# Performance work log

Measured on AMD Instinct MI355X. Metric: run time of the kernel, lower is better.

## Reference

```python
import jax, jax.numpy as jnp
import numpy as np

N_NODES = 100000
IN_DIM = 64
HIDDEN = 128
N_EDGES = 1000000


def _linear_params(key, fan_in, fan_out):
    # torch nn.Linear default init: U(-1/sqrt(fan_in), 1/sqrt(fan_in))
    kW, kb = jax.random.split(key)
    bound = 1.0 / np.sqrt(fan_in)
    W = jax.random.uniform(kW, (fan_in, fan_out), jnp.float32, -bound, bound)
    b = jax.random.uniform(kb, (fan_out,), jnp.float32, -bound, bound)
    return W, b


def setup_inputs() -> dict:
    key = jax.random.key(0)
    kx, ke, k1, k2, k3, k4 = jax.random.split(key, 6)
    x = jax.random.normal(kx, (N_NODES, IN_DIM), jnp.float32)
    edge_index = jax.random.randint(ke, (2, N_EDGES), 0, N_NODES, jnp.int64)
    W1, b1 = _linear_params(k1, IN_DIM * 2, HIDDEN)
    W2, b2 = _linear_params(k2, HIDDEN, HIDDEN)
    W3, b3 = _linear_params(k3, HIDDEN, HIDDEN)
    W4, b4 = _linear_params(k4, HIDDEN, 1)
    return {"x": x, "edge_index": edge_index,
            "W1": W1, "b1": b1, "W2": W2, "b2": b2,
            "W3": W3, "b3": b3, "W4": W4, "b4": b4}


def reference(x, edge_index, W1, b1, W2, b2, W3, b3, W4, b4):
    src, dst = edge_index[0], edge_index[1]
    # [E, 2*in_dim] gathered edge inputs
    edge_inputs = jnp.concatenate([x[src], x[dst]], axis=1)
    h = jnp.tanh(edge_inputs @ W1 + b1)
    h = jnp.tanh(h @ W2 + b2)
    h = jnp.tanh(h @ W3 + b3)
    out = jax.nn.sigmoid(h @ W4 + b4)
    return out.squeeze(-1)  # [E]
```

## Files before the change

kernel.cpp:

```cpp
#include <hip/hip_runtime.h>
#include <cstdint>

typedef _Float16 f16x8 __attribute__((ext_vector_type(8)));
typedef float    f32x4 __attribute__((ext_vector_type(4)));

#define E_TOTAL   1000000
#define N_NODES   100000
#define NROUNDS   3907
#define GRID_MAIN 512

__device__ __forceinline__ float fast_tanh(float x) {
  float e = __builtin_amdgcn_exp2f(x * 2.8853900817779268f);
  return 1.0f - 2.0f * __builtin_amdgcn_rcpf(1.0f + e);
}
__device__ __forceinline__ float fast_sigmoid(float x) {
  float e = __builtin_amdgcn_exp2f(x * -1.4426950408889634f);
  return __builtin_amdgcn_rcpf(1.0f + e);
}
__device__ __forceinline__ uint32_t pack2(float a, float b) {
  return __builtin_bit_cast(uint32_t, __builtin_amdgcn_cvt_pkrtz(a, b));
}
__device__ __forceinline__ f16x8 asfrag(const uint32_t (&u)[4]) {
  uint4 v;
  v.x = u[0]; v.y = u[1]; v.z = u[2]; v.w = u[3];
  return __builtin_bit_cast(f16x8, v);
}

__global__ void kconv_x(const float* __restrict__ x, _Float16* __restrict__ xh) {
  int i = blockIdx.x * 256 + threadIdx.x;
  if (i >= (N_NODES * 64) / 8) return;
  const float4* p = (const float4*)x + (size_t)i * 2;
  float4 a = p[0], b = p[1];
  f16x8 o = {(_Float16)a.x, (_Float16)a.y, (_Float16)a.z, (_Float16)a.w,
             (_Float16)b.x, (_Float16)b.y, (_Float16)b.z, (_Float16)b.w};
  *((f16x8*)xh + i) = o;
}

__global__ void kswz_w(const float* __restrict__ W1, const float* __restrict__ W2,
                       const float* __restrict__ W3, _Float16* __restrict__ wswz) {
  int idx = blockIdx.x * 256 + threadIdx.x;
  if (idx >= 49152) return;
  int jj = idx & 7;
  int l  = (idx >> 3) & 63;
  int s  = (idx >> 9) & 3;
  int T  = (idx >> 11) & 7;
  int L  = idx >> 14;
  int k  = 32 * s + 4 * (l >> 4) + (jj & 3) + 16 * (jj >> 2);
  int n  = 16 * T + (l & 15);
  const float* W = (L == 0) ? W1 : ((L == 1) ? W2 : W3);
  wswz[idx] = (_Float16)W[k * 128 + n];
}

template <int L>
__device__ __forceinline__ void mlp_layer(const _Float16* lds_w, const float* lds_b,
                                          int lane,
                                          const uint32_t (&Bin)[2][4][4],
                                          uint32_t (&Bout)[2][4][4]) {
  const int g = lane >> 4;
#pragma unroll
  for (int T = 0; T < 8; ++T) {
    const f32x4 bf = *(const f32x4*)(lds_b + L * 128 + T * 16 + g * 4);
    f32x4 acc0 = bf, acc1 = bf;
#pragma unroll
    for (int s = 0; s < 4; ++s) {
      const f16x8 W = *(const f16x8*)(lds_w + (size_t)(((L * 8 + T) * 4 + s) * 512) + lane * 8);
      acc0 = __builtin_amdgcn_mfma_f32_16x16x32_f16(W, asfrag(Bin[0][s]), acc0, 0, 0, 0);
      acc1 = __builtin_amdgcn_mfma_f32_16x16x32_f16(W, asfrag(Bin[1][s]), acc1, 0, 0, 0);
    }
    const int si = T >> 1, d = (T & 1) * 2;
    Bout[0][si][d]     = pack2(fast_tanh(acc0[0]), fast_tanh(acc0[1]));
    Bout[0][si][d + 1] = pack2(fast_tanh(acc0[2]), fast_tanh(acc0[3]));
    Bout[1][si][d]     = pack2(fast_tanh(acc1[0]), fast_tanh(acc1[1]));
    Bout[1][si][d + 1] = pack2(fast_tanh(acc1[2]), fast_tanh(acc1[3]));
  }
}

__device__ __forceinline__ void mlp_out(const _Float16* __restrict__ gw3,
                                        const float* lds_b,
                                        int lane,
                                        const uint32_t (&Bin)[2][4][4],
                                        float (&dot)[2]) {
  const int g = lane >> 4;
  dot[0] = dot[1] = 0.f;
#pragma unroll
  for (int T = 0; T < 8; ++T) {
    const f32x4 bf = *(const f32x4*)(lds_b + 256 + T * 16 + g * 4);
    const f32x4 wf = *(const f32x4*)(lds_b + 384 + T * 16 + g * 4);
    f32x4 acc0 = bf, acc1 = bf;
#pragma unroll
    for (int s = 0; s < 4; ++s) {
      const f16x8 W = *(const f16x8*)(gw3 + (size_t)((T * 4 + s) * 512) + lane * 8);
      acc0 = __builtin_amdgcn_mfma_f32_16x16x32_f16(W, asfrag(Bin[0][s]), acc0, 0, 0, 0);
      acc1 = __builtin_amdgcn_mfma_f32_16x16x32_f16(W, asfrag(Bin[1][s]), acc1, 0, 0, 0);
    }
    dot[0] += fast_tanh(acc0[0]) * wf[0] + fast_tanh(acc0[1]) * wf[1]
            + fast_tanh(acc0[2]) * wf[2] + fast_tanh(acc0[3]) * wf[3];
    dot[1] += fast_tanh(acc1[0]) * wf[0] + fast_tanh(acc1[1]) * wf[1]
            + fast_tanh(acc1[2]) * wf[2] + fast_tanh(acc1[3]) * wf[3];
  }
}

template <bool XH>
__global__ __launch_bounds__(512)
void edge_mlp(
    const int* __restrict__ eidx,
    const _Float16* __restrict__ xh,
    const float* __restrict__ xf,
    const _Float16* __restrict__ wswz,
    const float* __restrict__ b1, const float* __restrict__ b2,
    const float* __restrict__ b3, const float* __restrict__ w4,
    const float* __restrict__ b4g,
    float* __restrict__ out) {
  extern __shared__ char smem[];
  _Float16* lds_w = (_Float16*)smem;
  float*    lds_b = (float*)(smem + 65536);
  const _Float16* gw3 = wswz + 32768;

  const int tid = threadIdx.x;
  {
    const uint4* src = (const uint4*)wswz;
    uint4* dst = (uint4*)smem;
#pragma unroll
    for (int i = 0; i < 8; ++i) dst[tid + i * 512] = src[tid + i * 512];
  }
  if (tid < 128) {
    lds_b[tid]       = b1[tid];
    lds_b[128 + tid] = b2[tid];
    lds_b[256 + tid] = b3[tid];
    lds_b[384 + tid] = w4[tid];
  }
  __syncthreads();

  const float b4v = b4g[0];
  const int wid = tid >> 6, lane = tid & 63;
  const int c = lane & 15, g = lane >> 4;

  for (int round = blockIdx.x; round < NROUNDS; round += GRID_MAIN) {
    const int ebase = round * 256 + wid * 32;

    uint32_t B0[2][4][4];
#pragma unroll
    for (int t = 0; t < 2; ++t) {
      int e  = ebase + t * 16 + c;
      int ee = (e < E_TOTAL) ? e : 0;
      int sN = eidx[ee];
      int dN = eidx[E_TOTAL + ee];
      if (XH) {
        const _Float16* ps = xh + (size_t)sN * 64 + g * 4;
        const _Float16* pd = xh + (size_t)dN * 64 + g * 4;
#pragma unroll
        for (int sp = 0; sp < 2; ++sp) {
#pragma unroll
          for (int h = 0; h < 2; ++h) {
            uint2 rs = *(const uint2*)(ps + sp * 32 + h * 16);
            uint2 rd = *(const uint2*)(pd + sp * 32 + h * 16);
            B0[t][sp][h * 2]         = rs.x;
            B0[t][sp][h * 2 + 1]     = rs.y;
            B0[t][2 + sp][h * 2]     = rd.x;
            B0[t][2 + sp][h * 2 + 1] = rd.y;
          }
        }
      } else {
        const float* ps = xf + (size_t)sN * 64 + g * 4;
        const float* pd = xf + (size_t)dN * 64 + g * 4;
#pragma unroll
        for (int sp = 0; sp < 2; ++sp) {
#pragma unroll
          for (int h = 0; h < 2; ++h) {
            float4 fs = *(const float4*)(ps + sp * 32 + h * 16);
            float4 fd = *(const float4*)(pd + sp * 32 + h * 16);
            B0[t][sp][h * 2]         = pack2(fs.x, fs.y);
            B0[t][sp][h * 2 + 1]     = pack2(fs.z, fs.w);
            B0[t][2 + sp][h * 2]     = pack2(fd.x, fd.y);
            B0[t][2 + sp][h * 2 + 1] = pack2(fd.z, fd.w);
          }
        }
      }
    }

    uint32_t B1r[2][4][4], B2r[2][4][4];
    mlp_layer<0>(lds_w, lds_b, lane, B0, B1r);
    mlp_layer<1>(lds_w, lds_b, lane, B1r, B2r);

    float dot[2];
    mlp_out(gw3, lds_b, lane, B2r, dot);

#pragma unroll
    for (int t = 0; t < 2; ++t) {
      float v = dot[t];
      v += __shfl_xor(v, 16);
      v += __shfl_xor(v, 32);
      dot[t] = v;
    }
    if (g == 0) {
#pragma unroll
      for (int t = 0; t < 2; ++t) {
        int e = ebase + t * 16 + c;
        if (e < E_TOTAL) out[e] = fast_sigmoid(dot[t] + b4v);
      }
    }
    __builtin_amdgcn_sched_barrier(0);
  }
}

extern "C" void kernel_launch(void* const* d_in, const int* in_sizes, int n_in,
                              void* d_out, int out_size, void* d_ws, size_t ws_size,
                              hipStream_t stream) {
  (void)in_sizes; (void)n_in; (void)out_size;
  const float* x  = (const float*)d_in[0];
  const int* eidx = (const int*)d_in[1];
  const float* W1 = (const float*)d_in[2];
  const float* b1 = (const float*)d_in[3];
  const float* W2 = (const float*)d_in[4];
  const float* b2 = (const float*)d_in[5];
  const float* W3 = (const float*)d_in[6];
  const float* b3 = (const float*)d_in[7];
  const float* w4 = (const float*)d_in[8];
  const float* b4 = (const float*)d_in[9];
  float* out = (float*)d_out;

  const size_t XH_BYTES   = (size_t)N_NODES * 64 * 2;
  const size_t WS_W_BYTES = 49152 * 2;
  const bool xh_ok = ws_size >= XH_BYTES + WS_W_BYTES;

  _Float16* ws_xh = (_Float16*)d_ws;
  _Float16* ws_w  = (_Float16*)((char*)d_ws + (xh_ok ? XH_BYTES : 0));

  kswz_w<<<192, 256, 0, stream>>>(W1, W2, W3, ws_w);
  if (xh_ok) kconv_x<<<3125, 256, 0, stream>>>(x, ws_xh);

  const size_t lds_bytes = 65536 + 2048;
  if (xh_ok) {
    edge_mlp<true><<<GRID_MAIN, 512, lds_bytes, stream>>>(
        eidx, ws_xh, x, ws_w, b1, b2, b3, w4, b4, out);
  } else {
    edge_mlp<false><<<GRID_MAIN, 512, lds_bytes, stream>>>(
        eidx, ws_xh, x, ws_w, b1, b2, b3, w4, b4, out);
  }
}
```

Measured before the change: 164.0 us.

## Fold tanh scale into weights, halve block size, stream W2 from global

The tanh input scale factor is folded into the swizzled fp16 weights and the biases, so each activation skips one multiply. Blocks shrink from 512 to 256 threads and the grid doubles. LDS now holds only W1 (32KB), and W2 is read from global/L2 the way W3 already was, to fit more blocks per CU. The risk is that per-tile W2 loads from L2 cost more than the occupancy gain, and fp16 rounding of the prescaled weights changes slightly.

```diff
diff --git a/kernel.cpp b/kernel.cpp
--- a/kernel.cpp
+++ b/kernel.cpp
@@ -6,11 +6,12 @@
 
 #define E_TOTAL   1000000
 #define N_NODES   100000
-#define NROUNDS   3907
-#define GRID_MAIN 512
-
-__device__ __forceinline__ float fast_tanh(float x) {
-  float e = __builtin_amdgcn_exp2f(x * 2.8853900817779268f);
+#define NROUNDS   7813
+#define GRID_MAIN 1024
+#define SCL       2.8853900817779268f
+
+__device__ __forceinline__ float tanh_pre(float a) {
+  float e = __builtin_amdgcn_exp2f(a);
   return 1.0f - 2.0f * __builtin_amdgcn_rcpf(1.0f + e);
 }
 __device__ __forceinline__ float fast_sigmoid(float x) {
@@ -48,12 +49,12 @@
   int k  = 32 * s + 4 * (l >> 4) + (jj & 3) + 16 * (jj >> 2);
   int n  = 16 * T + (l & 15);
   const float* W = (L == 0) ? W1 : ((L == 1) ? W2 : W3);
-  wswz[idx] = (_Float16)W[k * 128 + n];
+  wswz[idx] = (_Float16)(W[k * 128 + n] * SCL);
 }
 
 template <int L>
-__device__ __forceinline__ void mlp_layer(const _Float16* lds_w, const float* lds_b,
-                                          int lane,
+__device__ __forceinline__ void mlp_layer(const _Float16* __restrict__ w,
+                                          const float* lds_b, int lane,
                                           const uint32_t (&Bin)[2][4][4],
                                           uint32_t (&Bout)[2][4][4]) {
   const int g = lane >> 4;
@@ -63,21 +64,20 @@
     f32x4 acc0 = bf, acc1 = bf;
 #pragma unroll
     for (int s = 0; s < 4; ++s) {
-      const f16x8 W = *(const f16x8*)(lds_w + (size_t)(((L * 8 + T) * 4 + s) * 512) + lane * 8);
+      const f16x8 W = *(const f16x8*)(w + (size_t)(((T * 4 + s)) * 512) + lane * 8);
       acc0 = __builtin_amdgcn_mfma_f32_16x16x32_f16(W, asfrag(Bin[0][s]), acc0, 0, 0, 0);
       acc1 = __builtin_amdgcn_mfma_f32_16x16x32_f16(W, asfrag(Bin[1][s]), acc1, 0, 0, 0);
     }
     const int si = T >> 1, d = (T & 1) * 2;
-    Bout[0][si][d]     = pack2(fast_tanh(acc0[0]), fast_tanh(acc0[1]));
-    Bout[0][si][d + 1] = pack2(fast_tanh(acc0[2]), fast_tanh(acc0[3]));
-    Bout[1][si][d]     = pack2(fast_tanh(acc1[0]), fast_tanh(acc1[1]));
-    Bout[1][si][d + 1] = pack2(fast_tanh(acc1[2]), fast_tanh(acc1[3]));
+    Bout[0][si][d]     = pack2(tanh_pre(acc0[0]), tanh_pre(acc0[1]));
+    Bout[0][si][d + 1] = pack2(tanh_pre(acc0[2]), tanh_pre(acc0[3]));
+    Bout[1][si][d]     = pack2(tanh_pre(acc1[0]), tanh_pre(acc1[1]));
+    Bout[1][si][d + 1] = pack2(tanh_pre(acc1[2]), tanh_pre(acc1[3]));
   }
 }
 
 __device__ __forceinline__ void mlp_out(const _Float16* __restrict__ gw3,
-                                        const float* lds_b,
-                                        int lane,
+                                        const float* lds_b, int lane,
                                         const uint32_t (&Bin)[2][4][4],
                                         float (&dot)[2]) {
   const int g = lane >> 4;
@@ -93,15 +93,15 @@
       acc0 = __builtin_amdgcn_mfma_f32_16x16x32_f16(W, asfrag(Bin[0][s]), acc0, 0, 0, 0);
       acc1 = __builtin_amdgcn_mfma_f32_16x16x32_f16(W, asfrag(Bin[1][s]), acc1, 0, 0, 0);
     }
-    dot[0] += fast_tanh(acc0[0]) * wf[0] + fast_tanh(acc0[1]) * wf[1]
-            + fast_tanh(acc0[2]) * wf[2] + fast_tanh(acc0[3]) * wf[3];
-    dot[1] += fast_tanh(acc1[0]) * wf[0] + fast_tanh(acc1[1]) * wf[1]
-            + fast_tanh(acc1[2]) * wf[2] + fast_tanh(acc1[3]) * wf[3];
+    dot[0] += tanh_pre(acc0[0]) * wf[0] + tanh_pre(acc0[1]) * wf[1]
+            + tanh_pre(acc0[2]) * wf[2] + tanh_pre(acc0[3]) * wf[3];
+    dot[1] += tanh_pre(acc1[0]) * wf[0] + tanh_pre(acc1[1]) * wf[1]
+            + tanh_pre(acc1[2]) * wf[2] + tanh_pre(acc1[3]) * wf[3];
   }
 }
 
 template <bool XH>
-__global__ __launch_bounds__(512)
+__global__ __launch_bounds__(256)
 void edge_mlp(
     const int* __restrict__ eidx,
     const _Float16* __restrict__ xh,
@@ -112,8 +112,9 @@
     const float* __restrict__ b4g,
     float* __restrict__ out) {
   extern __shared__ char smem[];
-  _Float16* lds_w = (_Float16*)smem;
-  float*    lds_b = (float*)(smem + 65536);
+  _Float16* lds_w1 = (_Float16*)smem;
+  float*    lds_b  = (float*)(smem + 32768);
+  const _Float16* gw2 = wswz + 16384;
   const _Float16* gw3 = wswz + 32768;
 
   const int tid = threadIdx.x;
@@ -121,12 +122,12 @@
     const uint4* src = (const uint4*)wswz;
     uint4* dst = (uint4*)smem;
 #pragma unroll
-    for (int i = 0; i < 8; ++i) dst[tid + i * 512] = src[tid + i * 512];
+    for (int i = 0; i < 8; ++i) dst[tid + i * 256] = src[tid + i * 256];
   }
   if (tid < 128) {
-    lds_b[tid]       = b1[tid];
-    lds_b[128 + tid] = b2[tid];
-    lds_b[256 + tid] = b3[tid];
+    lds_b[tid]       = b1[tid] * SCL;
+    lds_b[128 + tid] = b2[tid] * SCL;
+    lds_b[256 + tid] = b3[tid] * SCL;
     lds_b[384 + tid] = w4[tid];
   }
   __syncthreads();
@@ -136,7 +137,7 @@
   const int c = lane & 15, g = lane >> 4;
 
   for (int round = blockIdx.x; round < NROUNDS; round += GRID_MAIN) {
-    const int ebase = round * 256 + wid * 32;
+    const int ebase = round * 128 + wid * 32;
 
     uint32_t B0[2][4][4];
 #pragma unroll
@@ -179,8 +180,8 @@
     }
 
     uint32_t B1r[2][4][4], B2r[2][4][4];
-    mlp_layer<0>(lds_w, lds_b, lane, B0, B1r);
-    mlp_layer<1>(lds_w, lds_b, lane, B1r, B2r);
+    mlp_layer<0>(lds_w1, lds_b, lane, B0, B1r);
+    mlp_layer<1>(gw2,    lds_b, lane, B1r, B2r);
 
     float dot[2];
     mlp_out(gw3, lds_b, lane, B2r, dot);
@@ -229,12 +230,12 @@
   kswz_w<<<192, 256, 0, stream>>>(W1, W2, W3, ws_w);
   if (xh_ok) kconv_x<<<3125, 256, 0, stream>>>(x, ws_xh);
 
-  const size_t lds_bytes = 65536 + 2048;
+  const size_t lds_bytes = 32768 + 2048;
   if (xh_ok) {
-    edge_mlp<true><<<GRID_MAIN, 512, lds_bytes, stream>>>(
+    edge_mlp<true><<<GRID_MAIN, 256, lds_bytes, stream>>>(
         eidx, ws_xh, x, ws_w, b1, b2, b3, w4, b4, out);
   } else {
-    edge_mlp<false><<<GRID_MAIN, 512, lds_bytes, stream>>>(
+    edge_mlp<false><<<GRID_MAIN, 256, lds_bytes, stream>>>(
         eidx, ws_xh, x, ws_w, b1, b2, b3, w4, b4, out);
   }
 }
```

Result: slower. 250.2 us (+52.6%).
